# Kernel tuning notes

Hardware: AMD Instinct MI355X
Metric: run time of the kernel (lower is better)

The kernel has to match this reference:

```python
import jax, jax.numpy as jnp
import numpy as np
import math

B, T, C, NH, LEVEL = 2, 2048, 1024, 16, 3


def _build_sets(T, level):
    # hierarchical dyadic sets: levels `level`..floor(log2(T)), step 2^l
    sets = []
    levelmax = int(math.floor(math.log2(T)))
    for l in range(level, levelmax + 1):
        step = 2 ** l
        for i in range(T // step):
            sets.append((i * step, (i + 1) * step - 1))
    b = np.asarray(sets, dtype=np.int32)
    return b[:, 0], b[:, 1]


def setup_inputs() -> dict:
    key = jax.random.key(0)
    kx, kw1, kw2 = jax.random.split(key, 3)
    x = jax.random.normal(kx, (B, T, C), dtype=jnp.float32)
    # torch nn.Linear stores weight as (out_features, in_features); y = x @ W.T
    W_attn = jax.random.normal(kw1, (3 * C, C), dtype=jnp.float32) * (C ** -0.5)
    W_proj = jax.random.normal(kw2, (C, C), dtype=jnp.float32) * (C ** -0.5)
    return {"x": x, "W_attn": W_attn, "W_proj": W_proj}


def _get_slice(xc, l_idx, r_idx):
    # xc: (B,NH,T,hs) cumulative sums; returns sum over [l_idx, r_idx]
    r = xc[:, :, r_idx, :]
    l = xc[:, :, l_idx - 1, :] * (l_idx >= 1)[None, None, :, None].astype(xc.dtype)
    return r - l


def _forward(x, W_attn, W_proj):
    hs = C // NH
    scale = hs ** -0.5
    qkv = x @ W_attn.T                      # (B,T,3C)
    q, k, v = jnp.split(qkv, 3, axis=2)
    heads = lambda t: t.reshape(B, T, NH, hs).transpose(0, 2, 1, 3)  # (B,NH,T,hs)
    q, k, v = heads(q), heads(k), heads(v)
    phi = lambda t: jax.nn.elu(t) + 1.0     # feature_map = 'elu_plus'
    q_phi, k_phi = phi(q), phi(k)
    k_cum = jnp.cumsum(k_phi, axis=2)
    v_cum = jnp.cumsum(v, axis=2)

    l_np, r_np = _build_sets(T, LEVEL)
    l_idx, r_idx = jnp.asarray(l_np), jnp.asarray(r_np)
    K = _get_slice(k_cum, l_idx, r_idx)     # (B,NH,S,hs)
    V = _get_slice(v_cum, l_idx, r_idx)

    t_idx = jnp.arange(T)
    mask = t_idx[:, None] >= r_idx[None, :]                 # (T,S)
    logits = jnp.einsum('bhtd,bhsd->bhts', q, K) * scale    # raw q here (as in source)
    logits = jnp.where(mask[None, None], logits, -jnp.inf)

    # tail term over last (t mod 2^level)+1 tokens, uses q_phi
    Lmin = 2 ** LEVEL
    tail_len = t_idx % Lmin + 1
    l_tail = t_idx - tail_len + 1
    K_tail = _get_slice(k_cum, l_tail, t_idx)               # (B,NH,T,hs)
    V_tail = _get_slice(v_cum, l_tail, t_idx)
    tail_logit = jnp.sum(q_phi * K_tail, axis=-1) * scale   # (B,NH,T)

    full = jnp.concatenate([logits, tail_logit[..., None]], axis=-1)
    att = jax.nn.softmax(full, axis=-1)
    out = jnp.einsum('bhts,bhsd->bhtd', att[..., :-1], V) + att[..., -1:] * V_tail
    out = out.transpose(0, 2, 1, 3).reshape(B, T, C)
    return out @ W_proj.T


def reference(x, W_attn, W_proj):
    return _forward(x, W_attn, W_proj)
```

## Files before the change

kernel.cpp:

```cpp
#include <hip/hip_runtime.h>
#include <hip/hip_bf16.h>
#include <stdint.h>

#define B_    2
#define T_    2048
#define CD    1024
#define NH_   16
#define HS_   64
#define NSETS 511
#define NSP   512
#define QKV_LD 3072
#define NEGBIG (-3.4e38f)

typedef __attribute__((ext_vector_type(8))) short  short8;
typedef __attribute__((ext_vector_type(4))) float  f32x4;

__device__ __forceinline__ unsigned short f2bf(float f) {
  unsigned u = __float_as_uint(f);
  unsigned r = 0x7FFFu + ((u >> 16) & 1u);
  return (unsigned short)((u + r) >> 16);
}
__device__ __forceinline__ float bf2f(unsigned short h) {
  return __uint_as_float(((unsigned)h) << 16);
}
__device__ __forceinline__ float elu1(float x) {
  return x > 0.f ? x + 1.f : __expf(x);
}
__device__ __forceinline__ void gload16(const unsigned short* g, short* l) {
  __builtin_amdgcn_global_load_lds(
      (const __attribute__((address_space(1))) unsigned int*)g,
      (__attribute__((address_space(3))) unsigned int*)l, 16, 0, 0);
}

__global__ __launch_bounds__(256) void split3_kernel(
    const float* __restrict__ x, const float* __restrict__ Wa,
    const float* __restrict__ Wp,
    unsigned short* __restrict__ xh, unsigned short* __restrict__ xl,
    unsigned short* __restrict__ wah, unsigned short* __restrict__ wal,
    unsigned short* __restrict__ wph) {
  int bid = blockIdx.x;
  const float* src; unsigned short *hi, *lo; int base;
  if (bid < 16384)      { src = x;  hi = xh;  lo = xl;  base = bid; }
  else if (bid < 24576) { src = Wa; hi = wah; lo = wal; base = bid - 16384; }
  else if (bid < 28672) { src = Wa; hi = wah; lo = nullptr; base = bid - 16384; }
  else                  { src = Wp; hi = wph; lo = nullptr; base = bid - 28672; }
  int i = base * 256 + threadIdx.x;
  float v = src[i];
  unsigned short h = f2bf(v);
  hi[i] = h;
  if (lo) lo[i] = f2bf(v - bf2f(h));
}

template<int SPLIT>
__device__ __forceinline__ void gemm_body(
    short* lds,
    const unsigned short* __restrict__ Ah, const unsigned short* __restrict__ Al,
    const unsigned short* __restrict__ Bh, const unsigned short* __restrict__ Bl,
    float* __restrict__ Cmat, int K, int ldc, int row0, int col0)
{
  const int tid  = threadIdx.x;
  const int lane = tid & 63;
  const int w    = tid >> 6;
  const int wr   = w >> 1, wc = w & 1;

  f32x4 acc[4][4];
  #pragma unroll
  for (int a = 0; a < 4; ++a)
    #pragma unroll
    for (int b = 0; b < 4; ++b)
      acc[a][b] = (f32x4){0.f, 0.f, 0.f, 0.f};

  const int rlane = lane & 15;
  const int kgrp  = lane >> 4;
  const int rsw   = (kgrp ^ (rlane & 3) ^ ((rlane >> 2) & 3)) << 4;

  const int slr = lane >> 2;
  const int sch = (lane & 3) ^ (slr & 3) ^ ((slr >> 2) & 3);

  const unsigned short* ssrc;
  size_t srb;
  short* sbase;
  if (SPLIT) {
    ssrc = (w == 0) ? Ah : (w == 1) ? Bh : (w == 2) ? Al : Bl;
    srb  = (w & 1) ? (size_t)col0 : (size_t)row0;
    sbase = &lds[w * 4096];
  } else {
    ssrc = (w & 1) ? Bh : Ah;
    srb  = (w & 1) ? (size_t)col0 : (size_t)row0;
    sbase = &lds[(w & 1) * 4096 + (w >> 1) * 2048];
    srb += (size_t)(w >> 1) * 64;
  }

  for (int kt = 0; kt < K; kt += 32) {
    __syncthreads();
    const unsigned short* g0 = ssrc + (srb + slr) * K + kt + (sch << 3);
    if (SPLIT) {
      #pragma unroll
      for (int i = 0; i < 8; ++i)
        gload16(g0 + (size_t)i * 16 * K, sbase + i * 512);
    } else {
      #pragma unroll
      for (int i = 0; i < 4; ++i)
        gload16(g0 + (size_t)i * 16 * K, sbase + i * 512);
    }
    __syncthreads();

    short8 aH[4], bH[4], aL[4], bL[4];
    #pragma unroll
    for (int m = 0; m < 4; ++m) {
      int r    = wr * 64 + m * 16 + rlane;
      int cidx = wc * 64 + m * 16 + rlane;
      aH[m] = *(const short8*)((const char*)lds + r * 64 + rsw);
      bH[m] = *(const short8*)((const char*)lds + 8192 + cidx * 64 + rsw);
      if (SPLIT) {
        aL[m] = *(const short8*)((const char*)lds + 16384 + r * 64 + rsw);
        bL[m] = *(const short8*)((const char*)lds + 24576 + cidx * 64 + rsw);
      }
    }
    #pragma unroll
    for (int mm = 0; mm < 4; ++mm)
      #pragma unroll
      for (int nn = 0; nn < 4; ++nn) {
        acc[mm][nn] = __builtin_amdgcn_mfma_f32_16x16x32_bf16(aH[mm], bH[nn], acc[mm][nn], 0, 0, 0);
        if (SPLIT) {
          acc[mm][nn] = __builtin_amdgcn_mfma_f32_16x16x32_bf16(aH[mm], bL[nn], acc[mm][nn], 0, 0, 0);
          acc[mm][nn] = __builtin_amdgcn_mfma_f32_16x16x32_bf16(aL[mm], bH[nn], acc[mm][nn], 0, 0, 0);
        }
      }
  }

  const int rl = (lane >> 4) * 4;
  const int cl = lane & 15;
  #pragma unroll
  for (int mm = 0; mm < 4; ++mm)
    #pragma unroll
    for (int nn = 0; nn < 4; ++nn)
      #pragma unroll
      for (int r = 0; r < 4; ++r) {
        int row = row0 + wr * 64 + mm * 16 + rl + r;
        int col = col0 + wc * 64 + nn * 16 + cl;
        Cmat[(size_t)row * ldc + col] = acc[mm][nn][r];
      }
}

template<int SPLIT>
__global__ __launch_bounds__(256) void gemm_bt(
    const unsigned short* __restrict__ Ah, const unsigned short* __restrict__ Al,
    const unsigned short* __restrict__ Bh, const unsigned short* __restrict__ Bl,
    float* __restrict__ Cmat, int M, int N, int K, int ldc)
{
  constexpr int NT = SPLIT ? 4 : 2;
  __shared__ short lds[NT * 4096];
  const int nwg = gridDim.x;
  const int cpx = nwg >> 3;
  const int bid = blockIdx.x;
  const int swb = (bid & 7) * cpx + (bid >> 3);
  const int nbx = N >> 7;
  const int bx = swb % nbx;
  const int by = swb / nbx;
  gemm_body<SPLIT>(lds, Ah, Al, Bh, Bl, Cmat, K, ldc, by * 128, bx * 128);
}

__global__ __launch_bounds__(256) void cs_part(const float* __restrict__ qkv,
                                               float* __restrict__ part) {
  int blk = blockIdx.x;
  int q   = blk & 1;
  int seg = (blk >> 1) & 63;
  int b   = blk >> 7;
  int c   = threadIdx.x * 4;
  const float* src = qkv + (size_t)(b * T_ + seg * 32) * QKV_LD + CD + q * CD + c;
  float4 s = {0.f, 0.f, 0.f, 0.f};
  #pragma unroll 4
  for (int j = 0; j < 32; ++j) {
    float4 v = *(const float4*)(src + (size_t)j * QKV_LD);
    if (q == 0) {
      s.x += elu1(v.x); s.y += elu1(v.y); s.z += elu1(v.z); s.w += elu1(v.w);
    } else {
      s.x += v.x; s.y += v.y; s.z += v.z; s.w += v.w;
    }
  }
  *(float4*)(part + ((size_t)(b * 64 + seg) * 2048) + q * 1024 + c) = s;
}

__global__ __launch_bounds__(256) void cs_final(const float* __restrict__ qkv,
                                                const float* __restrict__ part,
                                                float* __restrict__ kcum,
                                                float* __restrict__ vcum) {
  int blk = blockIdx.x;
  int q   = blk & 1;
  int seg = (blk >> 1) & 63;
  int b   = blk >> 7;
  int c   = threadIdx.x * 4;
  int h   = c >> 6, d = c & 63;
  float4 s = {0.f, 0.f, 0.f, 0.f};
  const float* pb = part + (size_t)(b * 64) * 2048 + q * 1024 + c;
  #pragma unroll 8
  for (int ss = 0; ss < seg; ++ss) {
    float4 p = *(const float4*)(pb + (size_t)ss * 2048);
    s.x += p.x; s.y += p.y; s.z += p.z; s.w += p.w;
  }
  const float* src = qkv + (size_t)(b * T_ + seg * 32) * QKV_LD + CD + q * CD + c;
  float* dst = (q == 0 ? kcum : vcum) + ((size_t)(b * NH_ + h) * T_ + seg * 32) * HS_ + d;
  #pragma unroll 4
  for (int j = 0; j < 32; ++j) {
    float4 v = *(const float4*)(src + (size_t)j * QKV_LD);
    if (q == 0) {
      s.x += elu1(v.x); s.y += elu1(v.y); s.z += elu1(v.z); s.w += elu1(v.w);
    } else {
      s.x += v.x; s.y += v.y; s.z += v.z; s.w += v.w;
    }
    *(float4*)(dst + (size_t)j * HS_) = s;
  }
}

__global__ __launch_bounds__(256) void build_sets2(
    const float* __restrict__ kcum, const float* __restrict__ vcum,
    unsigned short* __restrict__ Ksh, unsigned short* __restrict__ Ksl,
    unsigned short* __restrict__ Vst, int* __restrict__ r_srt)
{
  __shared__ int   lr[64], lli[64];
  __shared__ float vt[64][65];
  const int bh = blockIdx.x >> 3;
  const int s0 = (blockIdx.x & 7) * 64;
  const int tid = threadIdx.x;

  for (int s = tid; s < NSP; s += 256) {
    int r, li, rank;
    if (s == NSETS) { r = 0x7fffffff; li = 0; rank = NSETS; }
    else {
      int lvl = 3, base = 0;
      while (s >= base + (T_ >> lvl)) { base += T_ >> lvl; ++lvl; }
      int i = s - base;
      int m = (i + 1) << lvl;
      r = m - 1; li = i << lvl;
      rank = lvl - 3;
      #pragma unroll
      for (int j = 3; j <= 11; ++j) rank += (m - 8) >> j;
    }
    if (rank >= s0 && rank < s0 + 64) {
      lr[rank - s0]  = r;
      lli[rank - s0] = li;
      if (bh == 0) r_srt[rank] = r;
    }
  }
  __syncthreads();

  const int sl = tid >> 2;
  const int dq = (tid & 3) * 16;
  const int r  = lr[sl], li = lli[sl];
  const size_t orow = ((size_t)(bh << 9) + s0 + sl) * HS_ + dq;
  short8 kh0, kh1, kl0, kl1;
  if (r == 0x7fffffff) {
    #pragma unroll
    for (int j = 0; j < 8; ++j) { kh0[j]=0; kh1[j]=0; kl0[j]=0; kl1[j]=0; }
    #pragma unroll
    for (int j = 0; j < 16; ++j) vt[sl][dq + j] = 0.f;
  } else {
    const float* kr0 = kcum + ((size_t)bh * T_ + r) * HS_ + dq;
    const float* vr0 = vcum + ((size_t)bh * T_ + r) * HS_ + dq;
    const float* kr1 = kcum + ((size_t)bh * T_ + (li - 1)) * HS_ + dq;
    const float* vr1 = vcum + ((size_t)bh * T_ + (li - 1)) * HS_ + dq;
    #pragma unroll
    for (int g = 0; g < 4; ++g) {
      float4 kv = *(const float4*)(kr0 + g * 4);
      float4 vv = *(const float4*)(vr0 + g * 4);
      if (li > 0) {
        float4 k1 = *(const float4*)(kr1 + g * 4);
        float4 v1 = *(const float4*)(vr1 + g * 4);
        kv.x -= k1.x; kv.y -= k1.y; kv.z -= k1.z; kv.w -= k1.w;
        vv.x -= v1.x; vv.y -= v1.y; vv.z -= v1.z; vv.w -= v1.w;
      }
      float ka[4] = {kv.x, kv.y, kv.z, kv.w};
      float va[4] = {vv.x, vv.y, vv.z, vv.w};
      #pragma unroll
      for (int j = 0; j < 4; ++j) {
        int e = g * 4 + j;
        unsigned short h = f2bf(ka[j]);
        unsigned short l = f2bf(ka[j] - bf2f(h));
        if (e < 8) { kh0[e] = (short)h; kl0[e] = (short)l; }
        else       { kh1[e - 8] = (short)h; kl1[e - 8] = (short)l; }
        vt[sl][dq + e] = va[j];
      }
    }
  }
  *(short8*)(Ksh + orow)     = kh0;
  *(short8*)(Ksh + orow + 8) = kh1;
  *(short8*)(Ksl + orow)     = kl0;
  *(short8*)(Ksl + orow + 8) = kl1;
  __syncthreads();

  const int d  = tid >> 2;
  const int sq = (tid & 3) * 16;
  short8 a, b2;
  #pragma unroll
  for (int j = 0; j < 8; ++j) {
    a[j]  = (short)f2bf(vt[sq + j][d]);
    b2[j] = (short)f2bf(vt[sq + 8 + j][d]);
  }
  unsigned short* dst = Vst + ((size_t)(bh << 6) + d) * NSP + s0 + sq;
  *(short8*)dst = a;
  *(short8*)(dst + 8) = b2;
}

__global__ __launch_bounds__(256) void attn_mfma(
    const float* __restrict__ qkv, const float* __restrict__ kcum,
    const float* __restrict__ vcum,
    const unsigned short* __restrict__ Ksh, const unsigned short* __restrict__ Ksl,
    const unsigned short* __restrict__ Vst, const int* __restrict__ r_srt,
    unsigned short* __restrict__ attnb)
{
  __shared__ short Pl[4 * 2048];
  __shared__ short KV[2][3 * 4096];
  __shared__ int   rs_lds[NSP];

  const int blk = blockIdx.x;
  const int xcd = blk & 7;
  const int j   = blk >> 3;
  const int bhx = j >> 4;
  const int bh  = xcd * 4 + bhx;
  const int rb  = ((j & 15) + bhx * 4) & 15;
  const int b = bh >> 4, h = bh & 15;
  const int t0 = rb * 128;
  const int tid = threadIdx.x;
  const int lane = tid & 63;
  const int w = tid >> 6;
  const int col = lane & 15;
  const int kgrp = (lane >> 4) * 8;
  const float scale = 0.125f;

  const int srow = lane >> 3;
  const int scsw = ((lane & 7) ^ srow) * 8;

  auto stage_tile = [&](short* kv, int s0) {
    #pragma unroll
    for (int L = w * 6; L < w * 6 + 6; ++L) {
      int a = L >> 3, i = L & 7;
      const unsigned short* src;
      if (a == 0)      src = Ksh + ((size_t)(bh << 9) + s0 + i * 8 + srow) * 64 + scsw;
      else if (a == 1) src = Ksl + ((size_t)(bh << 9) + s0 + i * 8 + srow) * 64 + scsw;
      else             src = Vst + ((size_t)(bh << 6) + i * 8 + srow) * NSP + s0 + scsw;
      gload16(src, kv + a * 4096 + i * 512 + lane * 8);
    }
  };

  short8 qh[2][2], ql[2][2];
  #pragma unroll
  for (int rr = 0; rr < 2; ++rr) {
    int qrow = t0 + w * 32 + rr * 16 + col;
    const float* qr = qkv + (size_t)(b * T_ + qrow) * QKV_LD + h * HS_;
    #pragma unroll
    for (int ks = 0; ks < 2; ++ks) {
      float4 v0 = *(const float4*)(qr + kgrp + ks * 32);
      float4 v1 = *(const float4*)(qr + kgrp + ks * 32 + 4);
      float vv[8] = {v0.x, v0.y, v0.z, v0.w, v1.x, v1.y, v1.z, v1.w};
      #pragma unroll
      for (int jj = 0; jj < 8; ++jj) {
        unsigned short hi = f2bf(vv[jj]);
        qh[rr][ks][jj] = (short)hi;
        ql[rr][ks][jj] = (short)f2bf(vv[jj] - bf2f(hi));
      }
    }
  }
  for (int s = tid; s < NSP; s += 256) rs_lds[s] = r_srt[s];
  stage_tile(&KV[0][0], 0);
  __syncthreads();

  int rows[2][4];
  #pragma unroll
  for (int rr = 0; rr < 2; ++rr)
    #pragma unroll
    for (int r = 0; r < 4; ++r)
      rows[rr][r] = t0 + w * 32 + rr * 16 + (lane >> 4) * 4 + r;

  f32x4 O[2][4];
  float mrun[2][4], lsum[2][4];
  #pragma unroll
  for (int rr = 0; rr < 2; ++rr)
    #pragma unroll
    for (int f = 0; f < 4; ++f) {
      O[rr][f] = (f32x4){0.f, 0.f, 0.f, 0.f};
      mrun[rr][f] = NEGBIG; lsum[rr][f] = 0.f;
    }

  int nmax = 0;
  #pragma unroll
  for (int jj = 3; jj <= 11; ++jj) nmax += (t0 + 128) >> jj;
  const int ntiles = (nmax + 63) >> 6;
  int cur = 0;

  for (int tile = 0; tile < ntiles; ++tile) {
    const int s0 = tile * 64;
    if (tile + 1 < ntiles) stage_tile(&KV[cur ^ 1][0], s0 + 64);

    const char* kc = (const char*)&KV[cur][0];
    f32x4 S[2][4];
    #pragma unroll
    for (int rr = 0; rr < 2; ++rr)
      #pragma unroll
      for (int f = 0; f < 4; ++f) S[rr][f] = (f32x4){0.f, 0.f, 0.f, 0.f};

    #pragma unroll
    for (int ks = 0; ks < 2; ++ks) {
      int chnk = (lane >> 4) + ks * 4;
      #pragma unroll
      for (int f = 0; f < 4; ++f) {
        int so = f * 16 + col;
        int kb = so * 128 + ((chnk ^ (so & 7)) << 4);
        short8 bHv = *(const short8*)(kc + kb);
        short8 bLv = *(const short8*)(kc + 8192 + kb);
        #pragma unroll
        for (int rr = 0; rr < 2; ++rr) {
          S[rr][f] = __builtin_amdgcn_mfma_f32_16x16x32_bf16(qh[rr][ks], bHv, S[rr][f], 0, 0, 0);
          S[rr][f] = __builtin_amdgcn_mfma_f32_16x16x32_bf16(qh[rr][ks], bLv, S[rr][f], 0, 0, 0);
          S[rr][f] = __builtin_amdgcn_mfma_f32_16x16x32_bf16(ql[rr][ks], bHv, S[rr][f], 0, 0, 0);
        }
      }
    }

    int rsv[4];
    #pragma unroll
    for (int f = 0; f < 4; ++f) rsv[f] = rs_lds[s0 + f * 16 + col];

    #pragma unroll
    for (int rr = 0; rr < 2; ++rr)
      #pragma unroll
      for (int f = 0; f < 4; ++f)
        #pragma unroll
        for (int r = 0; r < 4; ++r)
          S[rr][f][r] = (rsv[f] > rows[rr][r]) ? NEGBIG : S[rr][f][r] * scale;

    float mx[2][4];
    int pred = 1;
    #pragma unroll
    for (int rr = 0; rr < 2; ++rr)
      #pragma unroll
      for (int r = 0; r < 4; ++r) {
        mx[rr][r] = fmaxf(fmaxf(S[rr][0][r], S[rr][1][r]),
                          fmaxf(S[rr][2][r], S[rr][3][r]));
        pred &= (mx[rr][r] <= mrun[rr][r] + 8.f);
      }
    if (!__all(pred)) {
      #pragma unroll
      for (int rr = 0; rr < 2; ++rr)
        #pragma unroll
        for (int r = 0; r < 4; ++r) {
          float mt = mx[rr][r];
          mt = fmaxf(mt, __shfl_xor(mt, 1));
          mt = fmaxf(mt, __shfl_xor(mt, 2));
          mt = fmaxf(mt, __shfl_xor(mt, 4));
          mt = fmaxf(mt, __shfl_xor(mt, 8));
          float mv = fmaxf(mrun[rr][r], mt);
          float fs = __expf(mrun[rr][r] - mv);
          lsum[rr][r] *= fs;
          #pragma unroll
          for (int f = 0; f < 4; ++f) O[rr][f][r] *= fs;
          mrun[rr][r] = mv;
        }
    }

    char* pw = (char*)Pl + w * 4096;
    #pragma unroll
    for (int rr = 0; rr < 2; ++rr)
      #pragma unroll
      for (int r = 0; r < 4; ++r) {
        int rowr = rr * 16 + (lane >> 4) * 4 + r;
        int rswz = (rowr & 7) << 4;
        #pragma unroll
        for (int f = 0; f < 4; ++f) {
          float p = __expf(S[rr][f][r] - mrun[rr][r]);
          p = (rsv[f] > rows[rr][r]) ? 0.f : p;
          lsum[rr][r] += p;
          int addr = (rowr * 128 + (f * 16 + col) * 2) ^ rswz;
          *(unsigned short*)(pw + addr) = f2bf(p);
        }
      }

    #pragma unroll
    for (int ks = 0; ks < 2; ++ks) {
      int chnk = (lane >> 4) + ks * 4;
      int pb0 = (col * 128 + (kgrp + ks * 32) * 2) ^ ((col & 7) << 4);
      short8 pa0 = *(const short8*)(pw + pb0);
      short8 pa1 = *(const short8*)(pw + 2048 + pb0);
      #pragma unroll
      for (int f = 0; f < 4; ++f) {
        int dr = f * 16 + col;
        short8 bv = *(const short8*)(kc + 16384 + dr * 128 + ((chnk ^ (dr & 7)) << 4));
        O[0][f] = __builtin_amdgcn_mfma_f32_16x16x32_bf16(pa0, bv, O[0][f], 0, 0, 0);
        O[1][f] = __builtin_amdgcn_mfma_f32_16x16x32_bf16(pa1, bv, O[1][f], 0, 0, 0);
      }
    }

    __syncthreads();
    cur ^= 1;
  }

  float lrun[2][4];
  #pragma unroll
  for (int rr = 0; rr < 2; ++rr)
    #pragma unroll
    for (int r = 0; r < 4; ++r) {
      float l = lsum[rr][r];
      l += __shfl_xor(l, 1);
      l += __shfl_xor(l, 2);
      l += __shfl_xor(l, 4);
      l += __shfl_xor(l, 8);
      lrun[rr][r] = l;
    }

  float ztail[2];
  #pragma unroll
  for (int rr = 0; rr < 2; ++rr) {
    int trow = lane >> 2;
    int t = t0 + w * 32 + rr * 16 + trow;
    int d0 = (lane & 3) * 16;
    const float* qr = qkv + (size_t)(b * T_ + t) * QKV_LD + h * HS_ + d0;
    float qv[16];
    #pragma unroll
    for (int jj = 0; jj < 4; ++jj) {
      float4 v = *(const float4*)(qr + jj * 4);
      qv[jj*4+0] = v.x; qv[jj*4+1] = v.y; qv[jj*4+2] = v.z; qv[jj*4+3] = v.w;
    }
    int lt = t & ~7;
    const float* kc1 = kcum + ((size_t)bh * T_ + t) * HS_ + d0;
    float kt[16];
    if (lt > 0) {
      const float* kc0 = kcum + ((size_t)bh * T_ + (lt - 1)) * HS_ + d0;
      #pragma unroll
      for (int jj = 0; jj < 16; ++jj) kt[jj] = kc1[jj] - kc0[jj];
    } else {
      #pragma unroll
      for (int jj = 0; jj < 16; ++jj) kt[jj] = kc1[jj];
    }
    float z = 0.f;
    #pragma unroll
    for (int jj = 0; jj < 16; ++jj) {
      float qp = qv[jj] > 0.f ? qv[jj] + 1.f : __expf(qv[jj]);
      z += qp * kt[jj];
    }
    z += __shfl_xor(z, 1);
    z += __shfl_xor(z, 2);
    ztail[rr] = z * scale;
  }

  #pragma unroll
  for (int rr = 0; rr < 2; ++rr)
    #pragma unroll
    for (int r = 0; r < 4; ++r) {
      float zt = __shfl(ztail[rr], ((lane >> 4) * 4 + r) * 4);
      float mv = fmaxf(mrun[rr][r], zt);
      float fs = __expf(mrun[rr][r] - mv);
      float pwgt = __expf(zt - mv);
      lrun[rr][r] = lrun[rr][r] * fs + pwgt;
      int tr = rows[rr][r];
      int ltr = tr & ~7;
      #pragma unroll
      for (int f = 0; f < 4; ++f) {
        int d = f * 16 + col;
        float v1 = vcum[((size_t)bh * T_ + tr) * HS_ + d];
        float vt = (ltr > 0) ? v1 - vcum[((size_t)bh * T_ + (ltr - 1)) * HS_ + d] : v1;
        O[rr][f][r] = O[rr][f][r] * fs + pwgt * vt;
      }
    }

  #pragma unroll
  for (int rr = 0; rr < 2; ++rr)
    #pragma unroll
    for (int r = 0; r < 4; ++r) {
      float inv = 1.f / lrun[rr][r];
      unsigned short* orow = attnb + (size_t)(b * T_ + rows[rr][r]) * CD + h * HS_;
      #pragma unroll
      for (int f = 0; f < 4; ++f)
        orow[f * 16 + col] = f2bf(O[rr][f][r] * inv);
    }
}

extern "C" void kernel_launch(void* const* d_in, const int* in_sizes, int n_in,
                              void* d_out, int out_size, void* d_ws, size_t ws_size,
                              hipStream_t stream) {
  const float* x  = (const float*)d_in[0];
  const float* Wa = (const float*)d_in[1];
  const float* Wp = (const float*)d_in[2];
  float* out = (float*)d_out;

  char* ws = (char*)d_ws;
  size_t off = 0;
  auto alloc = [&](size_t bytes) -> char* {
    char* p = ws + off;
    off += (bytes + 255) & ~(size_t)255;
    return p;
  };

  const int M = B_ * T_;
  float* qkv  = (float*)alloc((size_t)M * QKV_LD * 4);
  float* kcum = (float*)alloc((size_t)B_ * NH_ * T_ * HS_ * 4);
  float* vcum = (float*)alloc((size_t)B_ * NH_ * T_ * HS_ * 4);
  float* part = (float*)alloc((size_t)B_ * 64 * 2048 * 4);
  unsigned short* wph = (unsigned short*)alloc((size_t)CD * CD * 2);

  char* regionA = alloc((size_t)16777216);
  unsigned short* xh = (unsigned short*)regionA;
  unsigned short* xl = (unsigned short*)(regionA + (size_t)M * CD * 2);
  const size_t SETS_ELEMS = (size_t)B_ * NH_ * NSP * HS_;
  unsigned short* Ksh = (unsigned short*)regionA;
  unsigned short* Ksl = Ksh + SETS_ELEMS;
  unsigned short* Vst = (unsigned short*)(regionA + 2 * SETS_ELEMS * 2);
  int*            r_srt = (int*)(regionA + 3 * SETS_ELEMS * 2);

  char* regionB = alloc((size_t)12582912);
  unsigned short* wah = (unsigned short*)regionB;
  unsigned short* wal = (unsigned short*)(regionB + (size_t)3 * CD * CD * 2);
  unsigned short* attnb = (unsigned short*)regionB;

  split3_kernel<<<dim3(32768), dim3(256), 0, stream>>>(
      x, Wa, Wp, xh, xl, wah, wal, wph);

  gemm_bt<1><<<dim3((2048 / 128) * (M / 128)), dim3(256), 0, stream>>>(
      xh, xl, wah, wal, qkv, M, 2048, CD, QKV_LD);

  gemm_bt<0><<<dim3((1024 / 128) * (M / 128)), dim3(256), 0, stream>>>(
      xh, (const unsigned short*)nullptr, wah + (size_t)2048 * CD,
      (const unsigned short*)nullptr, qkv + 2048, M, 1024, CD, QKV_LD);

  cs_part<<<dim3(B_ * 64 * 2), dim3(256), 0, stream>>>(qkv, part);
  cs_final<<<dim3(B_ * 64 * 2), dim3(256), 0, stream>>>(qkv, part, kcum, vcum);

  build_sets2<<<dim3(B_ * NH_ * 8), dim3(256), 0, stream>>>(
      kcum, vcum, Ksh, Ksl, Vst, r_srt);

  attn_mfma<<<dim3(512), dim3(256), 0, stream>>>(
      qkv, kcum, vcum, Ksh, Ksl, Vst, r_srt, attnb);

  gemm_bt<0><<<dim3((CD / 128) * (M / 128)), dim3(256), 0, stream>>>(
      attnb, (const unsigned short*)nullptr, wph, (const unsigned short*)nullptr,
      out, M, CD, CD, CD);
}
```

Baseline: 230.1 us.

## Halve attention query tile to 64 rows and drop KV double buffering

The attention kernel now gives each block 64 query rows (16 per wave) instead of 128, so twice as many blocks are launched and causal tile counts become finer-grained. The KV tile is single-buffered with a sync before compute instead of prefetching the next tile, which roughly halves LDS use and register pressure per block. The aim is better occupancy and load balance across CUs. In exchange, each set tile is loaded twice as often across blocks, and global-load latency is no longer overlapped with compute inside a block.

```diff
diff --git a/kernel.cpp b/kernel.cpp
--- a/kernel.cpp
+++ b/kernel.cpp
@@ -309,18 +309,17 @@
     const unsigned short* __restrict__ Vst, const int* __restrict__ r_srt,
     unsigned short* __restrict__ attnb)
 {
-  __shared__ short Pl[4 * 2048];
-  __shared__ short KV[2][3 * 4096];
+  __shared__ short Pl[4 * 1024];
+  __shared__ short KV[3 * 4096];
   __shared__ int   rs_lds[NSP];
 
   const int blk = blockIdx.x;
   const int xcd = blk & 7;
   const int j   = blk >> 3;
-  const int bhx = j >> 4;
-  const int bh  = xcd * 4 + bhx;
-  const int rb  = ((j & 15) + bhx * 4) & 15;
+  const int bh  = xcd * 4 + (j >> 5);
+  const int tch = (j + ((j >> 5) << 3)) & 31;
   const int b = bh >> 4, h = bh & 15;
-  const int t0 = rb * 128;
+  const int t0 = tch * 64;
   const int tid = threadIdx.x;
   const int lane = tid & 63;
   const int w = tid >> 6;
@@ -331,7 +330,7 @@
   const int srow = lane >> 3;
   const int scsw = ((lane & 7) ^ srow) * 8;
 
-  auto stage_tile = [&](short* kv, int s0) {
+  auto stage_tile = [&](int s0) {
     #pragma unroll
     for (int L = w * 6; L < w * 6 + 6; ++L) {
       int a = L >> 3, i = L & 7;
@@ -339,14 +338,13 @@
       if (a == 0)      src = Ksh + ((size_t)(bh << 9) + s0 + i * 8 + srow) * 64 + scsw;
       else if (a == 1) src = Ksl + ((size_t)(bh << 9) + s0 + i * 8 + srow) * 64 + scsw;
       else             src = Vst + ((size_t)(bh << 6) + i * 8 + srow) * NSP + s0 + scsw;
-      gload16(src, kv + a * 4096 + i * 512 + lane * 8);
+      gload16(src, KV + a * 4096 + i * 512 + lane * 8);
     }
   };
 
-  short8 qh[2][2], ql[2][2];
-  #pragma unroll
-  for (int rr = 0; rr < 2; ++rr) {
-    int qrow = t0 + w * 32 + rr * 16 + col;
+  short8 qh[2], ql[2];
+  {
+    int qrow = t0 + w * 16 + col;
     const float* qr = qkv + (size_t)(b * T_ + qrow) * QKV_LD + h * HS_;
     #pragma unroll
     for (int ks = 0; ks < 2; ++ks) {
@@ -356,48 +354,39 @@
       #pragma unroll
       for (int jj = 0; jj < 8; ++jj) {
         unsigned short hi = f2bf(vv[jj]);
-        qh[rr][ks][jj] = (short)hi;
-        ql[rr][ks][jj] = (short)f2bf(vv[jj] - bf2f(hi));
+        qh[ks][jj] = (short)hi;
+        ql[ks][jj] = (short)f2bf(vv[jj] - bf2f(hi));
       }
     }
   }
   for (int s = tid; s < NSP; s += 256) rs_lds[s] = r_srt[s];
-  stage_tile(&KV[0][0], 0);
-  __syncthreads();
-
-  int rows[2][4];
-  #pragma unroll
-  for (int rr = 0; rr < 2; ++rr)
-    #pragma unroll
-    for (int r = 0; r < 4; ++r)
-      rows[rr][r] = t0 + w * 32 + rr * 16 + (lane >> 4) * 4 + r;
-
-  f32x4 O[2][4];
-  float mrun[2][4], lsum[2][4];
-  #pragma unroll
-  for (int rr = 0; rr < 2; ++rr)
-    #pragma unroll
-    for (int f = 0; f < 4; ++f) {
-      O[rr][f] = (f32x4){0.f, 0.f, 0.f, 0.f};
-      mrun[rr][f] = NEGBIG; lsum[rr][f] = 0.f;
-    }
+
+  int rows[4];
+  #pragma unroll
+  for (int r = 0; r < 4; ++r) rows[r] = t0 + w * 16 + (lane >> 4) * 4 + r;
+
+  f32x4 O[4];
+  float mrun[4], lsum[4];
+  #pragma unroll
+  for (int f = 0; f < 4; ++f) {
+    O[f] = (f32x4){0.f, 0.f, 0.f, 0.f};
+    mrun[f] = NEGBIG; lsum[f] = 0.f;
+  }
 
   int nmax = 0;
   #pragma unroll
-  for (int jj = 3; jj <= 11; ++jj) nmax += (t0 + 128) >> jj;
+  for (int jj = 3; jj <= 11; ++jj) nmax += (t0 + 64) >> jj;
   const int ntiles = (nmax + 63) >> 6;
-  int cur = 0;
 
   for (int tile = 0; tile < ntiles; ++tile) {
     const int s0 = tile * 64;
-    if (tile + 1 < ntiles) stage_tile(&KV[cur ^ 1][0], s0 + 64);
-
-    const char* kc = (const char*)&KV[cur][0];
-    f32x4 S[2][4];
-    #pragma unroll
-    for (int rr = 0; rr < 2; ++rr)
-      #pragma unroll
-      for (int f = 0; f < 4; ++f) S[rr][f] = (f32x4){0.f, 0.f, 0.f, 0.f};
+    stage_tile(s0);
+    __syncthreads();
+
+    const char* kc = (const char*)KV;
+    f32x4 S[4];
+    #pragma unroll
+    for (int f = 0; f < 4; ++f) S[f] = (f32x4){0.f, 0.f, 0.f, 0.f};
 
     #pragma unroll
     for (int ks = 0; ks < 2; ++ks) {
@@ -408,110 +397,92 @@
         int kb = so * 128 + ((chnk ^ (so & 7)) << 4);
         short8 bHv = *(const short8*)(kc + kb);
         short8 bLv = *(const short8*)(kc + 8192 + kb);
+        S[f] = __builtin_amdgcn_mfma_f32_16x16x32_bf16(qh[ks], bHv, S[f], 0, 0, 0);
+        S[f] = __builtin_amdgcn_mfma_f32_16x16x32_bf16(qh[ks], bLv, S[f], 0, 0, 0);
+        S[f] = __builtin_amdgcn_mfma_f32_16x16x32_bf16(ql[ks], bHv, S[f], 0, 0, 0);
+      }
+    }
+
+    int rsv[4];
+    #pragma unroll
+    for (int f = 0; f < 4; ++f) rsv[f] = rs_lds[s0 + f * 16 + col];
+
+    float zv[4][4];
+    #pragma unroll
+    for (int f = 0; f < 4; ++f)
+      #pragma unroll
+      for (int r = 0; r < 4; ++r)
+        zv[f][r] = (rsv[f] > rows[r]) ? NEGBIG : S[f][r] * scale;
+
+    float mx[4];
+    #pragma unroll
+    for (int r = 0; r < 4; ++r)
+      mx[r] = fmaxf(fmaxf(zv[0][r], zv[1][r]), fmaxf(zv[2][r], zv[3][r]));
+    int pred = (mx[0] <= mrun[0] + 8.f) & (mx[1] <= mrun[1] + 8.f) &
+               (mx[2] <= mrun[2] + 8.f) & (mx[3] <= mrun[3] + 8.f);
+    if (!__all(pred)) {
+      #pragma unroll
+      for (int r = 0; r < 4; ++r) {
+        float mt = mx[r];
+        mt = fmaxf(mt, __shfl_xor(mt, 1));
+        mt = fmaxf(mt, __shfl_xor(mt, 2));
+        mt = fmaxf(mt, __shfl_xor(mt, 4));
+        mt = fmaxf(mt, __shfl_xor(mt, 8));
+        float mv = fmaxf(mrun[r], mt);
+        float fs = __expf(mrun[r] - mv);
+        lsum[r] *= fs;
         #pragma unroll
-        for (int rr = 0; rr < 2; ++rr) {
-          S[rr][f] = __builtin_amdgcn_mfma_f32_16x16x32_bf16(qh[rr][ks], bHv, S[rr][f], 0, 0, 0);
-          S[rr][f] = __builtin_amdgcn_mfma_f32_16x16x32_bf16(qh[rr][ks], bLv, S[rr][f], 0, 0, 0);
-          S[rr][f] = __builtin_amdgcn_mfma_f32_16x16x32_bf16(ql[rr][ks], bHv, S[rr][f], 0, 0, 0);
-        }
-      }
-    }
-
-    int rsv[4];
-    #pragma unroll
-    for (int f = 0; f < 4; ++f) rsv[f] = rs_lds[s0 + f * 16 + col];
-
-    #pragma unroll
-    for (int rr = 0; rr < 2; ++rr)
-      #pragma unroll
-      for (int f = 0; f < 4; ++f)
-        #pragma unroll
-        for (int r = 0; r < 4; ++r)
-          S[rr][f][r] = (rsv[f] > rows[rr][r]) ? NEGBIG : S[rr][f][r] * scale;
-
-    float mx[2][4];
-    int pred = 1;
-    #pragma unroll
-    for (int rr = 0; rr < 2; ++rr)
-      #pragma unroll
-      for (int r = 0; r < 4; ++r) {
-        mx[rr][r] = fmaxf(fmaxf(S[rr][0][r], S[rr][1][r]),
-                          fmaxf(S[rr][2][r], S[rr][3][r]));
-        pred &= (mx[rr][r] <= mrun[rr][r] + 8.f);
-      }
-    if (!__all(pred)) {
-      #pragma unroll
-      for (int rr = 0; rr < 2; ++rr)
-        #pragma unroll
-        for (int r = 0; r < 4; ++r) {
-          float mt = mx[rr][r];
-          mt = fmaxf(mt, __shfl_xor(mt, 1));
-          mt = fmaxf(mt, __shfl_xor(mt, 2));
-          mt = fmaxf(mt, __shfl_xor(mt, 4));
-          mt = fmaxf(mt, __shfl_xor(mt, 8));
-          float mv = fmaxf(mrun[rr][r], mt);
-          float fs = __expf(mrun[rr][r] - mv);
-          lsum[rr][r] *= fs;
-          #pragma unroll
-          for (int f = 0; f < 4; ++f) O[rr][f][r] *= fs;
-          mrun[rr][r] = mv;
-        }
-    }
-
-    char* pw = (char*)Pl + w * 4096;
-    #pragma unroll
-    for (int rr = 0; rr < 2; ++rr)
-      #pragma unroll
-      for (int r = 0; r < 4; ++r) {
-        int rowr = rr * 16 + (lane >> 4) * 4 + r;
-        int rswz = (rowr & 7) << 4;
-        #pragma unroll
-        for (int f = 0; f < 4; ++f) {
-          float p = __expf(S[rr][f][r] - mrun[rr][r]);
-          p = (rsv[f] > rows[rr][r]) ? 0.f : p;
-          lsum[rr][r] += p;
-          int addr = (rowr * 128 + (f * 16 + col) * 2) ^ rswz;
-          *(unsigned short*)(pw + addr) = f2bf(p);
-        }
-      }
+        for (int f = 0; f < 4; ++f) O[f][r] *= fs;
+        mrun[r] = mv;
+      }
+    }
+
+    char* pw = (char*)Pl + w * 2048;
+    #pragma unroll
+    for (int r = 0; r < 4; ++r) {
+      int rowr = (lane >> 4) * 4 + r;
+      int rswz = (rowr & 7) << 4;
+      #pragma unroll
+      for (int f = 0; f < 4; ++f) {
+        float p = __expf(zv[f][r] - mrun[r]);
+        p = (rsv[f] > rows[r]) ? 0.f : p;
+        lsum[r] += p;
+        int addr = (rowr * 128 + (f * 16 + col) * 2) ^ rswz;
+        *(unsigned short*)(pw + addr) = f2bf(p);
+      }
+    }
 
     #pragma unroll
     for (int ks = 0; ks < 2; ++ks) {
       int chnk = (lane >> 4) + ks * 4;
-      int pb0 = (col * 128 + (kgrp + ks * 32) * 2) ^ ((col & 7) << 4);
-      short8 pa0 = *(const short8*)(pw + pb0);
-      short8 pa1 = *(const short8*)(pw + 2048 + pb0);
+      int pbyte = (col * 128 + (kgrp + ks * 32) * 2) ^ ((col & 7) << 4);
+      short8 pa = *(const short8*)(pw + pbyte);
       #pragma unroll
       for (int f = 0; f < 4; ++f) {
         int dr = f * 16 + col;
         short8 bv = *(const short8*)(kc + 16384 + dr * 128 + ((chnk ^ (dr & 7)) << 4));
-        O[0][f] = __builtin_amdgcn_mfma_f32_16x16x32_bf16(pa0, bv, O[0][f], 0, 0, 0);
-        O[1][f] = __builtin_amdgcn_mfma_f32_16x16x32_bf16(pa1, bv, O[1][f], 0, 0, 0);
+        O[f] = __builtin_amdgcn_mfma_f32_16x16x32_bf16(pa, bv, O[f], 0, 0, 0);
       }
     }
 
     __syncthreads();
-    cur ^= 1;
-  }
-
-  float lrun[2][4];
-  #pragma unroll
-  for (int rr = 0; rr < 2; ++rr)
-    #pragma unroll
-    for (int r = 0; r < 4; ++r) {
-      float l = lsum[rr][r];
-      l += __shfl_xor(l, 1);
-      l += __shfl_xor(l, 2);
-      l += __shfl_xor(l, 4);
-      l += __shfl_xor(l, 8);
-      lrun[rr][r] = l;
-    }
-
-  float ztail[2];
-  #pragma unroll
-  for (int rr = 0; rr < 2; ++rr) {
+  }
+
+  float lrun[4];
+  #pragma unroll
+  for (int r = 0; r < 4; ++r) {
+    float l = lsum[r];
+    l += __shfl_xor(l, 1);
+    l += __shfl_xor(l, 2);
+    l += __shfl_xor(l, 4);
+    l += __shfl_xor(l, 8);
+    lrun[r] = l;
+  }
+
+  float ztail;
+  {
     int trow = lane >> 2;
-    int t = t0 + w * 32 + rr * 16 + trow;
+    int t = t0 + w * 16 + trow;
     int d0 = (lane & 3) * 16;
     const float* qr = qkv + (size_t)(b * T_ + t) * QKV_LD + h * HS_ + d0;
     float qv[16];
@@ -539,39 +510,35 @@
     }
     z += __shfl_xor(z, 1);
     z += __shfl_xor(z, 2);
-    ztail[rr] = z * scale;
-  }
-
-  #pragma unroll
-  for (int rr = 0; rr < 2; ++rr)
-    #pragma unroll
-    for (int r = 0; r < 4; ++r) {
-      float zt = __shfl(ztail[rr], ((lane >> 4) * 4 + r) * 4);
-      float mv = fmaxf(mrun[rr][r], zt);
-      float fs = __expf(mrun[rr][r] - mv);
-      float pwgt = __expf(zt - mv);
-      lrun[rr][r] = lrun[rr][r] * fs + pwgt;
-      int tr = rows[rr][r];
-      int ltr = tr & ~7;
-      #pragma unroll
-      for (int f = 0; f < 4; ++f) {
-        int d = f * 16 + col;
-        float v1 = vcum[((size_t)bh * T_ + tr) * HS_ + d];
-        float vt = (ltr > 0) ? v1 - vcum[((size_t)bh * T_ + (ltr - 1)) * HS_ + d] : v1;
-        O[rr][f][r] = O[rr][f][r] * fs + pwgt * vt;
-      }
-    }
-
-  #pragma unroll
-  for (int rr = 0; rr < 2; ++rr)
-    #pragma unroll
-    for (int r = 0; r < 4; ++r) {
-      float inv = 1.f / lrun[rr][r];
-      unsigned short* orow = attnb + (size_t)(b * T_ + rows[rr][r]) * CD + h * HS_;
-      #pragma unroll
-      for (int f = 0; f < 4; ++f)
-        orow[f * 16 + col] = f2bf(O[rr][f][r] * inv);
-    }
+    ztail = z * scale;
+  }
+
+  #pragma unroll
+  for (int r = 0; r < 4; ++r) {
+    float zt = __shfl(ztail, ((lane >> 4) * 4 + r) * 4);
+    float mv = fmaxf(mrun[r], zt);
+    float fs = __expf(mrun[r] - mv);
+    float pwgt = __expf(zt - mv);
+    lrun[r] = lrun[r] * fs + pwgt;
+    int tr = rows[r];
+    int ltr = tr & ~7;
+    #pragma unroll
+    for (int f = 0; f < 4; ++f) {
+      int d = f * 16 + col;
+      float v1 = vcum[((size_t)bh * T_ + tr) * HS_ + d];
+      float vt = (ltr > 0) ? v1 - vcum[((size_t)bh * T_ + (ltr - 1)) * HS_ + d] : v1;
+      O[f][r] = O[f][r] * fs + pwgt * vt;
+    }
+  }
+
+  #pragma unroll
+  for (int r = 0; r < 4; ++r) {
+    float inv = 1.f / lrun[r];
+    unsigned short* orow = attnb + (size_t)(b * T_ + rows[r]) * CD + h * HS_;
+    #pragma unroll
+    for (int f = 0; f < 4; ++f)
+      orow[f * 16 + col] = f2bf(O[f][r] * inv);
+  }
 }
 
 extern "C" void kernel_launch(void* const* d_in, const int* in_sizes, int n_in,
@@ -627,7 +594,7 @@
   build_sets2<<<dim3(B_ * NH_ * 8), dim3(256), 0, stream>>>(
       kcum, vcum, Ksh, Ksl, Vst, r_srt);
 
-  attn_mfma<<<dim3(512), dim3(256), 0, stream>>>(
+  attn_mfma<<<dim3(1024), dim3(256), 0, stream>>>(
       qkv, kcum, vcum, Ksh, Ksl, Vst, r_srt, attnb);
 
   gemm_bt<0><<<dim3((CD / 128) * (M / 128)), dim3(256), 0, stream>>>(
```

New measurement: 203.9 us. 11.4% less time.
